# Kernel optimization log

Measured on AMD Instinct MI355X. Metric: run time of the kernel, lower is better.

Reference implementation:

```python
import jax, jax.numpy as jnp
import numpy as np

N = 4096      # number of nodes (len(batch_node))
K = 8         # number of adjacency channels
C = 256       # in_channels == out_channels
E = 131072    # number of edges (avg degree 32)


def setup_inputs() -> dict:
    key = jax.random.key(0)
    k1, k2, k3 = jax.random.split(key, 3)
    h = jax.random.normal(k1, (C, N), dtype=jnp.float32)
    X = jax.random.normal(k2, (E, K), dtype=jnp.float32)
    # sample unique (src, dst) pairs so the scatter-set has no duplicate writes
    rng = np.random.default_rng(0)
    flat = rng.choice(N * N, size=E, replace=False)
    edge_index = jnp.asarray(np.stack([flat // N, flat % N]).astype(np.int32))
    batch_node = jnp.zeros((N,), dtype=jnp.float32)
    # glorot uniform: stdv = sqrt(6 / (in + out))
    stdv = np.sqrt(6.0 / (C + C)).astype(np.float32)
    weight = jax.random.uniform(k3, (K, C, C), dtype=jnp.float32,
                                minval=-stdv, maxval=stdv)
    bias = jnp.zeros((C,), dtype=jnp.float32)
    return {"h": h, "X": X, "edge_index": edge_index,
            "batch_node": batch_node, "weight": weight, "bias": bias}


def reference(h, X, edge_index, batch_node, weight, bias):
    Kk = weight.shape[0]
    Nn = batch_node.shape[0]
    # scatter edge features into K dense [N, N] adjacency tensors
    resx = jnp.zeros((Kk, Nn, Nn), dtype=h.dtype)
    resx = resx.at[:, edge_index[0], edge_index[1]].set(X.T)
    # res[k] = h @ resx[k] : [K, C, N]
    res = jnp.einsum('cn,knm->kcm', h, resx)
    # sum_k weight[k] @ res[k] : [C, N]  (in_channels == out_channels)
    out = jnp.einsum('kio,kon->in', weight, res)
    # (res.T + bias).T == res + bias[:, None]
    return out + bias[:, None]
```

## Files before the change

kernel.cpp:

```cpp
#include <hip/hip_runtime.h>

constexpr int NN = 4096;
constexpr int KC = 8;
constexpr int CC = 256;
constexpr int NE = 131072;
constexpr int KK = KC * CC;
constexpr int CAP = 96;

typedef short bf16x8 __attribute__((ext_vector_type(8)));
typedef float f32x4 __attribute__((ext_vector_type(4)));

__device__ inline unsigned short f2bf(float f) {
    union { float f; unsigned int u; } v; v.f = f;
    unsigned int u = v.u;
    u += 0x7fffu + ((u >> 16) & 1u);
    return (unsigned short)(u >> 16);
}
__device__ inline float bf2f(unsigned short u) {
    union { unsigned int i; float f; } w; w.i = ((unsigned int)u) << 16; return w.f;
}

__global__ __launch_bounds__(256) void k_prep(
    const float* __restrict__ h, const float* __restrict__ w,
    unsigned short* __restrict__ ht, unsigned short* __restrict__ A,
    int* __restrict__ cursor) {
    int b = blockIdx.x;
    int t = threadIdx.x;
    if (b < 1024) {
        __shared__ float tile[32][33];
        int nb = b >> 3, cb = b & 7;
        int n0 = nb * 32, c0 = cb * 32;
        int tx = t & 31, ty = t >> 5;
#pragma unroll
        for (int j = 0; j < 32; j += 8)
            tile[ty + j][tx] = h[(size_t)(c0 + ty + j) * NN + n0 + tx];
        __syncthreads();
#pragma unroll
        for (int j = 0; j < 32; j += 8)
            ht[(size_t)(n0 + ty + j) * CC + c0 + tx] = f2bf(tile[tx][ty + j]);
    } else {
        int g = (b - 1024) * 256 + t;
        if (g < NN) cursor[g] = 0;
        int idx = g * 4;
        int o = idx & 255, k = (idx >> 8) & 7, i = idx >> 11;
        float4 wv = *reinterpret_cast<const float4*>(w + ((k << 16) | (i << 8) | o));
        ushort4 av;
        av.x = f2bf(wv.x); av.y = f2bf(wv.y); av.z = f2bf(wv.z); av.w = f2bf(wv.w);
        *reinterpret_cast<ushort4*>(A + idx) = av;
    }
}

__global__ void k_fill(const int* __restrict__ edge_src, const int* __restrict__ edge_dst,
                       int* __restrict__ cursor, int2* __restrict__ bins) {
    int e = blockIdx.x * 256 + threadIdx.x;
    int d = edge_dst[e];
    int slot = atomicAdd(&cursor[d], 1);
    if (slot < CAP) bins[d * CAP + slot] = make_int2(e, edge_src[e]);
}

__device__ inline void agg_accum(f32x4 acc[KC], float4 v, float4 xa, float4 xb) {
    f32x4 vv = {v.x, v.y, v.z, v.w};
    acc[0] += xa.x * vv; acc[1] += xa.y * vv;
    acc[2] += xa.z * vv; acc[3] += xa.w * vv;
    acc[4] += xb.x * vv; acc[5] += xb.y * vv;
    acc[6] += xb.z * vv; acc[7] += xb.w * vv;
}

__global__ __launch_bounds__(256) void k_agg(
    const int* __restrict__ cursor, const int2* __restrict__ bins,
    const float* __restrict__ X, const unsigned short* __restrict__ ht,
    unsigned short* __restrict__ agg) {
    const int wid  = __builtin_amdgcn_readfirstlane(threadIdx.x >> 6);
    const int lane = threadIdx.x & 63;
    const int n = blockIdx.x * 4 + wid;
    int cnt = cursor[n];
    cnt = cnt > CAP ? CAP : cnt;
    const int p0 = n * CAP;
    const int p1 = p0 + cnt;
    const float4* X4 = reinterpret_cast<const float4*>(X);

    f32x4 acc[KC] = {};

    int p = p0;
    for (; p + 8 <= p1; p += 8) {
        const int4* b4 = reinterpret_cast<const int4*>(bins + p);
        int4 r0 = b4[0], r1 = b4[1], r2 = b4[2], r3 = b4[3];
        int es[8] = {r0.x, r0.z, r1.x, r1.z, r2.x, r2.z, r3.x, r3.z};
        int ss[8] = {r0.y, r0.w, r1.y, r1.w, r2.y, r2.w, r3.y, r3.w};
        ushort4 u[8];
#pragma unroll
        for (int j = 0; j < 8; ++j)
            u[j] = *(const ushort4*)(ht + (size_t)ss[j] * CC + 4 * lane);
#pragma unroll
        for (int j = 0; j < 8; ++j) {
            float4 v = {bf2f(u[j].x), bf2f(u[j].y), bf2f(u[j].z), bf2f(u[j].w)};
            agg_accum(acc, v, X4[es[j] * 2], X4[es[j] * 2 + 1]);
        }
    }
    for (; p < p1; ++p) {
        int2 q = bins[p];
        ushort4 u = *(const ushort4*)(ht + (size_t)q.y * CC + 4 * lane);
        float4 v = {bf2f(u.x), bf2f(u.y), bf2f(u.z), bf2f(u.w)};
        agg_accum(acc, v, X4[q.x * 2], X4[q.x * 2 + 1]);
    }

    unsigned short* op = agg + (size_t)n * KK + 4 * lane;
#pragma unroll
    for (int k = 0; k < KC; ++k) {
        ushort4 w;
        w.x = f2bf(acc[k][0]); w.y = f2bf(acc[k][1]);
        w.z = f2bf(acc[k][2]); w.w = f2bf(acc[k][3]);
        *reinterpret_cast<ushort4*>(op + k * CC) = w;
    }
}

__global__ __launch_bounds__(256) void k_gemm_mfma(
    const unsigned short* __restrict__ A, const unsigned short* __restrict__ B,
    const float* __restrict__ bias, float* __restrict__ out) {
    constexpr int BM = 64, BN = 32, BK = 64;
    constexpr int NT = KK / BK;
    __shared__ unsigned short As[4][BM][BK];
    __shared__ unsigned short Bs[4][BN][BK];
    const int tid  = threadIdx.x;
    const int wid  = tid >> 6;
    const int lane = tid & 63;

    const int raw = blockIdx.x;
    const int swz = (raw & 7) * 64 + (raw >> 3);
    const int i0 = (swz & 3) * BM;
    const int n0 = (swz >> 2) * BN;

    const int wm = (wid & 1) * 32;
    const int wn = (wid >> 1) * 16;

    const int lrow = lane >> 3;
    const int csrc = ((lane & 7) ^ lrow) * 8;

    f32x4 acc[2] = {};

#define STAGE(T, BUF)                                                              \
    do {                                                                           \
        int kc0_ = (T) * BK;                                                       \
        _Pragma("unroll")                                                          \
        for (int q = 0; q < 2; ++q) {                                              \
            int seg = wid + q * 4;                                                 \
            int row = seg * 8 + lrow;                                              \
            __builtin_amdgcn_global_load_lds(                                      \
                (const __attribute__((address_space(1))) void*)(                   \
                    A + (size_t)(i0 + row) * KK + kc0_ + csrc),                    \
            (__attribute__((address_space(3))) void*)(                             \
                    (char*)&As[BUF][0][0] + seg * 1024), 16, 0, 0);                \
        }                                                                          \
        {                                                                          \
            int row = wid * 8 + lrow;                                              \
            __builtin_amdgcn_global_load_lds(                                      \
                (const __attribute__((address_space(1))) void*)(                   \
                    B + (size_t)(n0 + row) * KK + kc0_ + csrc),                    \
                (__attribute__((address_space(3))) void*)(                         \
                    (char*)&Bs[BUF][0][0] + wid * 1024), 16, 0, 0);                \
        }                                                                          \
    } while (0)

    STAGE(0, 0);
    STAGE(1, 1);
    STAGE(2, 2);

    const int rA = wm + (lane & 15);
    const int rB = wn + (lane & 15);
    const int sw = lane & 7;
    const int chb = lane >> 4;

#pragma unroll
    for (int t = 0; t < NT; ++t) {
        if (t + 3 < NT) STAGE(t + 3, (t + 3) & 3);
        if (t + 3 < NT)      asm volatile("s_waitcnt vmcnt(9)" ::: "memory");
        else if (t + 2 < NT) asm volatile("s_waitcnt vmcnt(6)" ::: "memory");
        else if (t + 1 < NT) asm volatile("s_waitcnt vmcnt(3)" ::: "memory");
        else                 asm volatile("s_waitcnt vmcnt(0)" ::: "memory");
        __builtin_amdgcn_s_barrier();
        asm volatile("" ::: "memory");

        const char* Ab = (const char*)&As[t & 3][0][0];
        const char* Bb = (const char*)&Bs[t & 3][0][0];
#pragma unroll
        for (int ks = 0; ks < BK; ks += 32) {
            const int ch = (ks >> 3) + chb;
            bf16x8 a0 = *(const bf16x8*)(Ab + rA * 128 + ((ch ^ sw) << 4));
            bf16x8 a1 = *(const bf16x8*)(Ab + (rA + 16) * 128 + ((ch ^ sw) << 4));
            bf16x8 b0 = *(const bf16x8*)(Bb + rB * 128 + ((ch ^ sw) << 4));
            acc[0] = __builtin_amdgcn_mfma_f32_16x16x32_bf16(a0, b0, acc[0], 0, 0, 0);
            acc[1] = __builtin_amdgcn_mfma_f32_16x16x32_bf16(a1, b0, acc[1], 0, 0, 0);
        }
        asm volatile("" ::: "memory");
        __builtin_amdgcn_s_barrier();
    }
#undef STAGE

    const int lr = (lane >> 4) * 4;
    const int lc = lane & 15;
#pragma unroll
    for (int mi = 0; mi < 2; ++mi) {
#pragma unroll
        for (int r = 0; r < 4; ++r) {
            int i = i0 + wm + mi * 16 + lr + r;
            out[(size_t)i * NN + n0 + wn + lc] = acc[mi][r] + bias[i];
        }
    }
}

extern "C" void kernel_launch(void* const* d_in, const int* in_sizes, int n_in,
                              void* d_out, int out_size, void* d_ws, size_t ws_size,
                              hipStream_t stream) {
    const float* h      = (const float*)d_in[0];
    const float* X      = (const float*)d_in[1];
    const int* edge_idx = (const int*)d_in[2];
    const float* weight = (const float*)d_in[4];
    const float* bias   = (const float*)d_in[5];
    float* out = (float*)d_out;

    const int* edge_src = edge_idx;
    const int* edge_dst = edge_idx + NE;

    char* ws = (char*)d_ws;
    unsigned short* ht   = (unsigned short*)(ws);
    unsigned short* Abf  = (unsigned short*)(ws + (2 << 20));
    unsigned short* agg  = (unsigned short*)(ws + (4 << 20));
    size_t meta = (size_t)(20 << 20);
    int* cursor = (int*)(ws + meta);
    int2* bins  = (int2*)(ws + meta + 65536);

    k_prep<<<1536, 256, 0, stream>>>(h, weight, ht, Abf, cursor);
    k_fill<<<NE / 256, 256, 0, stream>>>(edge_src, edge_dst, cursor, bins);
    k_agg<<<NN / 4, 256, 0, stream>>>(cursor, bins, X, ht, agg);
    k_gemm_mfma<<<512, 256, 0, stream>>>(Abf, agg, bias, out);
}
```

Baseline: 56.08 us.

## Fuse edge aggregation and weight GEMM into one kernel via LDS staging

Merges the aggregation kernel and the MFMA GEMM into one kernel. Each 512-thread block aggregates 16 nodes, writes the bf16 aggregated features into swizzled LDS, then runs the 256x2048 weight GEMM for those 16 columns with A fragments loaded straight from global memory in registers and double-buffered. This removes the global round trip of the 16 MB aggregated intermediate and one kernel launch. In exchange there are only 256 blocks, and every block re-reads the full 1 MB weight matrix from global/L2 without LDS reuse, which risks low occupancy and high L2 traffic.

```diff
diff --git a/kernel.cpp b/kernel.cpp
--- a/kernel.cpp
+++ b/kernel.cpp
@@ -66,145 +66,111 @@
     acc[6] += xb.z * vv; acc[7] += xb.w * vv;
 }
 
-__global__ __launch_bounds__(256) void k_agg(
+__global__ __launch_bounds__(512) void k_fused(
     const int* __restrict__ cursor, const int2* __restrict__ bins,
     const float* __restrict__ X, const unsigned short* __restrict__ ht,
-    unsigned short* __restrict__ agg) {
+    const unsigned short* __restrict__ A, const float* __restrict__ bias,
+    float* __restrict__ out) {
+    __shared__ unsigned short Bs[16 * 2048];
+    char* BsB = (char*)Bs;
+    const int b    = blockIdx.x;
     const int wid  = __builtin_amdgcn_readfirstlane(threadIdx.x >> 6);
     const int lane = threadIdx.x & 63;
-    const int n = blockIdx.x * 4 + wid;
-    int cnt = cursor[n];
-    cnt = cnt > CAP ? CAP : cnt;
-    const int p0 = n * CAP;
-    const int p1 = p0 + cnt;
     const float4* X4 = reinterpret_cast<const float4*>(X);
 
-    f32x4 acc[KC] = {};
-
-    int p = p0;
-    for (; p + 8 <= p1; p += 8) {
-        const int4* b4 = reinterpret_cast<const int4*>(bins + p);
-        int4 r0 = b4[0], r1 = b4[1], r2 = b4[2], r3 = b4[3];
-        int es[8] = {r0.x, r0.z, r1.x, r1.z, r2.x, r2.z, r3.x, r3.z};
-        int ss[8] = {r0.y, r0.w, r1.y, r1.w, r2.y, r2.w, r3.y, r3.w};
-        ushort4 u[8];
-#pragma unroll
-        for (int j = 0; j < 8; ++j)
-            u[j] = *(const ushort4*)(ht + (size_t)ss[j] * CC + 4 * lane);
-#pragma unroll
-        for (int j = 0; j < 8; ++j) {
-            float4 v = {bf2f(u[j].x), bf2f(u[j].y), bf2f(u[j].z), bf2f(u[j].w)};
-            agg_accum(acc, v, X4[es[j] * 2], X4[es[j] * 2 + 1]);
+    for (int nn = 0; nn < 2; ++nn) {
+        const int nloc = wid * 2 + nn;
+        const int n = b * 16 + nloc;
+        int cnt = cursor[n];
+        cnt = cnt > CAP ? CAP : cnt;
+        const int p0 = n * CAP;
+        const int p1 = p0 + cnt;
+
+        f32x4 acc[KC] = {};
+        int p = p0;
+        for (; p + 8 <= p1; p += 8) {
+            const int4* b4 = reinterpret_cast<const int4*>(bins + p);
+            int4 r0 = b4[0], r1 = b4[1], r2 = b4[2], r3 = b4[3];
+            int es[8] = {r0.x, r0.z, r1.x, r1.z, r2.x, r2.z, r3.x, r3.z};
+            int ss[8] = {r0.y, r0.w, r1.y, r1.w, r2.y, r2.w, r3.y, r3.w};
+            ushort4 u[8];
+#pragma unroll
+            for (int j = 0; j < 8; ++j)
+                u[j] = *(const ushort4*)(ht + (size_t)ss[j] * CC + 4 * lane);
+#pragma unroll
+            for (int j = 0; j < 8; ++j) {
+                float4 v = {bf2f(u[j].x), bf2f(u[j].y), bf2f(u[j].z), bf2f(u[j].w)};
+                agg_accum(acc, v, X4[es[j] * 2], X4[es[j] * 2 + 1]);
+            }
         }
-    }
-    for (; p < p1; ++p) {
-        int2 q = bins[p];
-        ushort4 u = *(const ushort4*)(ht + (size_t)q.y * CC + 4 * lane);
-        float4 v = {bf2f(u.x), bf2f(u.y), bf2f(u.z), bf2f(u.w)};
-        agg_accum(acc, v, X4[q.x * 2], X4[q.x * 2 + 1]);
-    }
-
-    unsigned short* op = agg + (size_t)n * KK + 4 * lane;
-#pragma unroll
-    for (int k = 0; k < KC; ++k) {
-        ushort4 w;
-        w.x = f2bf(acc[k][0]); w.y = f2bf(acc[k][1]);
-        w.z = f2bf(acc[k][2]); w.w = f2bf(acc[k][3]);
-        *reinterpret_cast<ushort4*>(op + k * CC) = w;
-    }
-}
-
-__global__ __launch_bounds__(256) void k_gemm_mfma(
-    const unsigned short* __restrict__ A, const unsigned short* __restrict__ B,
-    const float* __restrict__ bias, float* __restrict__ out) {
-    constexpr int BM = 64, BN = 32, BK = 64;
-    constexpr int NT = KK / BK;
-    __shared__ unsigned short As[4][BM][BK];
-    __shared__ unsigned short Bs[4][BN][BK];
-    const int tid  = threadIdx.x;
-    const int wid  = tid >> 6;
-    const int lane = tid & 63;
-
-    const int raw = blockIdx.x;
-    const int swz = (raw & 7) * 64 + (raw >> 3);
-    const int i0 = (swz & 3) * BM;
-    const int n0 = (swz >> 2) * BN;
-
-    const int wm = (wid & 1) * 32;
-    const int wn = (wid >> 1) * 16;
-
-    const int lrow = lane >> 3;
-    const int csrc = ((lane & 7) ^ lrow) * 8;
-
-    f32x4 acc[2] = {};
-
-#define STAGE(T, BUF)                                                              \
-    do {                                                                           \
-        int kc0_ = (T) * BK;                                                       \
-        _Pragma("unroll")                                                          \
-        for (int q = 0; q < 2; ++q) {                                              \
-            int seg = wid + q * 4;                                                 \
-            int row = seg * 8 + lrow;                                              \
-            __builtin_amdgcn_global_load_lds(                                      \
-                (const __attribute__((address_space(1))) void*)(                   \
-                    A + (size_t)(i0 + row) * KK + kc0_ + csrc),                    \
-            (__attribute__((address_space(3))) void*)(                             \
-                    (char*)&As[BUF][0][0] + seg * 1024), 16, 0, 0);                \
-        }                                                                          \
-        {                                                                          \
-            int row = wid * 8 + lrow;                                              \
-            __builtin_amdgcn_global_load_lds(                                      \
-                (const __attribute__((address_space(1))) void*)(                   \
-                    B + (size_t)(n0 + row) * KK + kc0_ + csrc),                    \
-                (__attribute__((address_space(3))) void*)(                         \
-                    (char*)&Bs[BUF][0][0] + wid * 1024), 16, 0, 0);                \
-        }                                                                          \
+        for (; p < p1; ++p) {
+            int2 q = bins[p];
+            ushort4 u = *(const ushort4*)(ht + (size_t)q.y * CC + 4 * lane);
+            float4 v = {bf2f(u.x), bf2f(u.y), bf2f(u.z), bf2f(u.w)};
+            agg_accum(acc, v, X4[q.x * 2], X4[q.x * 2 + 1]);
+        }
+
+        const unsigned base = nloc * 4096 + 8 * lane;
+        const unsigned sx   = (nloc & 7) << 4;
+#pragma unroll
+        for (int k = 0; k < KC; ++k) {
+            ushort4 wv;
+            wv.x = f2bf(acc[k][0]); wv.y = f2bf(acc[k][1]);
+            wv.z = f2bf(acc[k][2]); wv.w = f2bf(acc[k][3]);
+            *reinterpret_cast<ushort4*>(BsB + ((base + k * 512) ^ sx)) = wv;
+        }
+    }
+    __syncthreads();
+
+    const int rA0 = wid * 32 + (lane & 15);
+    const int rA1 = rA0 + 16;
+    const int kq  = (lane >> 4) * 8;
+    const int brow = lane & 15;
+    const unsigned bbase = brow * 4096;
+    const unsigned bxor  = (brow & 7) << 4;
+
+    f32x4 acc0 = {}, acc1 = {};
+    bf16x8 ax0[4], ax1[4], ay0[4], ay1[4];
+
+#define LOADA(D0, D1, C0)                                                       \
+    _Pragma("unroll")                                                           \
+    for (int s = 0; s < 4; ++s) {                                               \
+        D0[s] = *(const bf16x8*)(A + (size_t)rA0 * KK + (C0) + s * 32 + kq);    \
+        D1[s] = *(const bf16x8*)(A + (size_t)rA1 * KK + (C0) + s * 32 + kq);    \
+    }
+#define DOCHUNK(S0, S1, C0)                                                     \
+    do {                                                                        \
+        bf16x8 bfr[4];                                                          \
+        _Pragma("unroll")                                                       \
+        for (int s = 0; s < 4; ++s) {                                           \
+            unsigned boff = (bbase + ((C0) + s * 32 + kq) * 2) ^ bxor;          \
+            bfr[s] = *(const bf16x8*)(BsB + boff);                              \
+        }                                                                       \
+        _Pragma("unroll")                                                       \
+        for (int s = 0; s < 4; ++s) {                                           \
+            acc0 = __builtin_amdgcn_mfma_f32_16x16x32_bf16(S0[s], bfr[s], acc0, 0, 0, 0); \
+            acc1 = __builtin_amdgcn_mfma_f32_16x16x32_bf16(S1[s], bfr[s], acc1, 0, 0, 0); \
+        }                                                                       \
     } while (0)
 
-    STAGE(0, 0);
-    STAGE(1, 1);
-    STAGE(2, 2);
-
-    const int rA = wm + (lane & 15);
-    const int rB = wn + (lane & 15);
-    const int sw = lane & 7;
-    const int chb = lane >> 4;
-
-#pragma unroll
-    for (int t = 0; t < NT; ++t) {
-        if (t + 3 < NT) STAGE(t + 3, (t + 3) & 3);
-        if (t + 3 < NT)      asm volatile("s_waitcnt vmcnt(9)" ::: "memory");
-        else if (t + 2 < NT) asm volatile("s_waitcnt vmcnt(6)" ::: "memory");
-        else if (t + 1 < NT) asm volatile("s_waitcnt vmcnt(3)" ::: "memory");
-        else                 asm volatile("s_waitcnt vmcnt(0)" ::: "memory");
-        __builtin_amdgcn_s_barrier();
-        asm volatile("" ::: "memory");
-
-        const char* Ab = (const char*)&As[t & 3][0][0];
-        const char* Bb = (const char*)&Bs[t & 3][0][0];
-#pragma unroll
-        for (int ks = 0; ks < BK; ks += 32) {
-            const int ch = (ks >> 3) + chb;
-            bf16x8 a0 = *(const bf16x8*)(Ab + rA * 128 + ((ch ^ sw) << 4));
-            bf16x8 a1 = *(const bf16x8*)(Ab + (rA + 16) * 128 + ((ch ^ sw) << 4));
-            bf16x8 b0 = *(const bf16x8*)(Bb + rB * 128 + ((ch ^ sw) << 4));
-            acc[0] = __builtin_amdgcn_mfma_f32_16x16x32_bf16(a0, b0, acc[0], 0, 0, 0);
-            acc[1] = __builtin_amdgcn_mfma_f32_16x16x32_bf16(a1, b0, acc[1], 0, 0, 0);
-        }
-        asm volatile("" ::: "memory");
-        __builtin_amdgcn_s_barrier();
-    }
-#undef STAGE
+    LOADA(ax0, ax1, 0);
+#pragma unroll
+    for (int c = 0; c < 16; c += 2) {
+        if (c + 1 < 16) LOADA(ay0, ay1, (c + 1) * 128);
+        DOCHUNK(ax0, ax1, c * 128);
+        if (c + 2 < 16) LOADA(ax0, ax1, (c + 2) * 128);
+        DOCHUNK(ay0, ay1, (c + 1) * 128);
+    }
+#undef LOADA
+#undef DOCHUNK
 
     const int lr = (lane >> 4) * 4;
     const int lc = lane & 15;
 #pragma unroll
-    for (int mi = 0; mi < 2; ++mi) {
-#pragma unroll
-        for (int r = 0; r < 4; ++r) {
-            int i = i0 + wm + mi * 16 + lr + r;
-            out[(size_t)i * NN + n0 + wn + lc] = acc[mi][r] + bias[i];
-        }
+    for (int r = 0; r < 4; ++r) {
+        int i = rA0 - (lane & 15) + lr + r;
+        out[(size_t)i * NN + b * 16 + lc] = acc0[r] + bias[i];
+        out[(size_t)(i + 16) * NN + b * 16 + lc] = acc1[r] + bias[i + 16];
     }
 }
 
@@ -224,13 +190,11 @@
     char* ws = (char*)d_ws;
     unsigned short* ht   = (unsigned short*)(ws);
     unsigned short* Abf  = (unsigned short*)(ws + (2 << 20));
-    unsigned short* agg  = (unsigned short*)(ws + (4 << 20));
-    size_t meta = (size_t)(20 << 20);
+    size_t meta = (size_t)(4 << 20);
     int* cursor = (int*)(ws + meta);
     int2* bins  = (int2*)(ws + meta + 65536);
 
     k_prep<<<1536, 256, 0, stream>>>(h, weight, ht, Abf, cursor);
     k_fill<<<NE / 256, 256, 0, stream>>>(edge_src, edge_dst, cursor, bins);
-    k_agg<<<NN / 4, 256, 0, stream>>>(cursor, bins, X, ht, agg);
-    k_gemm_mfma<<<512, 256, 0, stream>>>(Abf, agg, bias, out);
-}
+    k_fused<<<256, 512, 0, stream>>>(cursor, bins, X, ht, Abf, bias, out);
+}
```

Result: slower. 71.30 us (+27.1%).
